# Performance work log

Hardware: AMD Instinct MI355X
Metric: run time of the kernel (lower is better)

Reference implementation:

```python
import jax, jax.numpy as jnp
import numpy as np

D_MODEL = 1024
N_EXPERTS = 8
TOP_K = 2
D_HIDDEN = 4 * D_MODEL


def setup_inputs() -> dict:
    key = jax.random.key(0)
    ks = jax.random.split(key, 6)
    x = jax.random.normal(ks[0], (4, 2048, D_MODEL), dtype=jnp.float32)
    gate_w = jax.random.normal(ks[1], (N_EXPERTS, D_MODEL), dtype=jnp.float32) * 0.02
    w1 = jax.random.normal(ks[2], (N_EXPERTS, D_MODEL, D_HIDDEN), dtype=jnp.float32) * 0.02
    b1 = jnp.zeros((N_EXPERTS, D_HIDDEN), dtype=jnp.float32)
    w2 = jax.random.normal(ks[3], (N_EXPERTS, D_HIDDEN, D_MODEL), dtype=jnp.float32) * 0.02
    b2 = jnp.zeros((N_EXPERTS, D_MODEL), dtype=jnp.float32)
    return {"x": x, "gate_w": gate_w, "w1": w1, "b1": b1, "w2": w2, "b2": b2}


def reference(x, gate_w, w1, b1, w2, b2):
    B, S, D = x.shape
    xf = x.reshape(-1, D)                               # [T, D]
    logits = xf @ gate_w.T                              # [T, E]
    top_vals, top_idx = jax.lax.top_k(logits, TOP_K)    # [T, K]
    rw = jax.nn.softmax(top_vals.astype(jnp.float32), axis=-1).astype(x.dtype)  # [T, K]
    out = jnp.zeros_like(xf)
    for i in range(N_EXPERTS):
        # combined routing weight for expert i per token (0 if not selected)
        cw = jnp.sum(jnp.where(top_idx == i, rw, jnp.zeros_like(rw)), axis=-1)  # [T]
        h = jax.nn.relu(xf @ w1[i] + b1[i])             # [T, 4D]
        y = h @ w2[i] + b2[i]                           # [T, D]
        out = out + y * cw[:, None]
    return out.reshape(B, S, D)
```

## Files before the change

### kernel.cpp

```cpp
#include <hip/hip_runtime.h>
#include <stdint.h>

#define D_MODEL   1024
#define N_EXPERTS 8
#define D_HIDDEN  4096
#define T_TOKENS  8192
#define N_SLOTS   (T_TOKENS * 2)
#define MAX_MT    71

typedef __bf16 bf16x8 __attribute__((ext_vector_type(8)));
typedef float  f32x4  __attribute__((ext_vector_type(4)));
typedef unsigned short ushort8 __attribute__((ext_vector_type(8)));

__device__ __forceinline__ unsigned short f2bf(float f) {
    unsigned int u = __float_as_uint(f);
    u += 0x7fffu + ((u >> 16) & 1u);
    return (unsigned short)(u >> 16);
}
__device__ __forceinline__ float bf2f(unsigned short v) {
    return __uint_as_float((unsigned int)v << 16);
}

__device__ __forceinline__ void gl_lds16(const void* g, void* l) {
    __builtin_amdgcn_global_load_lds(
        (const __attribute__((address_space(1))) unsigned int*)g,
        (__attribute__((address_space(3))) unsigned int*)l, 16, 0, 0);
}

__global__ __launch_bounds__(256) void gate_kernel(
    const float* __restrict__ x, const float* __restrict__ gw,
    unsigned short* __restrict__ xb,
    int* __restrict__ route_pack, float* __restrict__ route_w,
    int* __restrict__ cnt)
{
    __shared__ float gws[N_EXPERTS * D_MODEL];
    __shared__ int hist[N_EXPERTS];
    int tid = threadIdx.x;
    for (int i = tid * 4; i < N_EXPERTS * D_MODEL; i += 256 * 4)
        *(float4*)&gws[i] = *(const float4*)&gw[i];
    if (tid < N_EXPERTS) hist[tid] = 0;
    __syncthreads();

    int wave = tid >> 6, lane = tid & 63;
    for (int tt = 0; tt < 4; tt++) {
        int t = blockIdx.x * 16 + wave * 4 + tt;
        const float* xr = x + (size_t)t * D_MODEL;

        float acc[N_EXPERTS];
        for (int e = 0; e < N_EXPERTS; e++) acc[e] = 0.f;
        for (int i = 0; i < 4; i++) {
            float4 xv = *(const float4*)&xr[lane * 4 + i * 256];
            ushort4 o;
            o.x = f2bf(xv.x); o.y = f2bf(xv.y); o.z = f2bf(xv.z); o.w = f2bf(xv.w);
            *(ushort4*)&xb[(size_t)t * D_MODEL + lane * 4 + i * 256] = o;
            for (int e = 0; e < N_EXPERTS; e++) {
                float4 gv = *(const float4*)&gws[e * D_MODEL + lane * 4 + i * 256];
                acc[e] += xv.x * gv.x + xv.y * gv.y + xv.z * gv.z + xv.w * gv.w;
            }
        }
        for (int e = 0; e < N_EXPERTS; e++)
            for (int off = 32; off >= 1; off >>= 1)
                acc[e] += __shfl_xor(acc[e], off, 64);

        if (lane == 0) {
            int e0 = 0; float v0 = acc[0];
            for (int e = 1; e < N_EXPERTS; e++) if (acc[e] > v0) { v0 = acc[e]; e0 = e; }
            int e1 = (e0 == 0) ? 1 : 0; float v1 = acc[e1];
            for (int e = 0; e < N_EXPERTS; e++)
                if (e != e0 && acc[e] > v1) { v1 = acc[e]; e1 = e; }
            float w0 = 1.f / (1.f + __expf(v1 - v0));
            route_pack[t] = e0 | (e1 << 8);
            route_w[2 * t]     = w0;
            route_w[2 * t + 1] = 1.f - w0;
            atomicAdd(&hist[e0], 1);
            atomicAdd(&hist[e1], 1);
        }
    }
    __syncthreads();
    if (tid < N_EXPERTS) atomicAdd(&cnt[tid], hist[tid]);
}

__global__ void offsets_kernel(const int* __restrict__ cnt,
                               int* __restrict__ off, int* __restrict__ cnt2)
{
    if (threadIdx.x == 0) {
        int a = 0;
        for (int e = 0; e < N_EXPERTS; e++) { off[e] = a; a += cnt[e]; cnt2[e] = 0; }
        off[N_EXPERTS] = a;
    }
}

__global__ __launch_bounds__(64) void scatter_kernel(
    const int* __restrict__ route_pack, const int* __restrict__ off,
    int* __restrict__ cnt2, int* __restrict__ tok_id, int* __restrict__ inv)
{
    int lane = threadIdx.x;
    int t = blockIdx.x * 64 + lane;
    int p  = route_pack[t];
    int e0 = p & 0xff, e1 = (p >> 8) & 0xff;

    unsigned long long m0[N_EXPERTS], m1[N_EXPERTS];
    for (int e = 0; e < N_EXPERTS; e++) {
        m0[e] = __ballot(e0 == e);
        m1[e] = __ballot(e1 == e);
    }
    int mybase = 0;
    if (lane < N_EXPERTS)
        mybase = atomicAdd(&cnt2[lane], __popcll(m0[lane]) + __popcll(m1[lane]));

    unsigned long long lt = (1ull << lane) - 1ull;
    int b0 = __shfl(mybase, e0);
    int s0 = off[e0] + b0 + (int)__popcll(m0[e0] & lt);
    int b1 = __shfl(mybase, e1);
    int s1 = off[e1] + b1 + (int)__popcll(m0[e1]) + (int)__popcll(m1[e1] & lt);

    tok_id[s0] = t;
    tok_id[s1] = t;
    inv[2 * t]     = s0;
    inv[2 * t + 1] = s1;
}

template <int R, int C>
__global__ __launch_bounds__(256) void transpose_convert_kernel(
    const float* __restrict__ src, unsigned short* __restrict__ dst)
{
    __shared__ float tile[64 * 68];
    int e = blockIdx.z;
    const float* s = src + (size_t)e * R * C;
    unsigned short* d = dst + (size_t)e * R * C;
    int r0 = blockIdx.y * 64, c0 = blockIdx.x * 64;
    int t = threadIdx.x;
    {
        int r = t >> 4, c4 = (t & 15) * 4;
        for (int p = 0; p < 4; p++, r += 16)
            *(float4*)&tile[r * 68 + c4] = *(const float4*)&s[(size_t)(r0 + r) * C + c0 + c4];
    }
    __syncthreads();
    {
        int c = t >> 2, rblk = (t & 3) * 8;
        for (int q = 0; q < 2; q++) {
            int rr = q * 32 + rblk;
            ushort8 o;
            for (int j = 0; j < 8; j++) o[j] = f2bf(tile[(rr + j) * 68 + c]);
            *(ushort8*)&d[(size_t)(c0 + c) * R + r0 + rr] = o;
        }
    }
}

template<int KDIM, int NC, bool RELU, bool USE_TOK>
__global__ __launch_bounds__(512, 2) void moe_gemm_kernel(
    const unsigned short* __restrict__ Ag, const unsigned short* __restrict__ Bw,
    const float* __restrict__ bias, const int* __restrict__ tok_id,
    const int* __restrict__ off, unsigned short* __restrict__ Cout)
{
    constexpr int NT   = KDIM / 64;
    constexpr int NTN  = NC / 256;
    constexpr int NWG  = MAX_MT * NTN;
    constexpr int ASH  = 256 * 64;
    constexpr int BUFS = 2 * ASH;
    __shared__ unsigned short smem[2 * BUFS];

    int wg = blockIdx.x;
    constexpr int qq8 = NWG / 8, rr8 = NWG % 8;
    int xcd = wg & 7, idx = wg >> 3;
    int sz = (xcd < rr8 ? xcd * (qq8 + 1) : rr8 * (qq8 + 1) + (xcd - rr8) * qq8) + idx;
    int bx = sz / NTN;
    int n0 = (sz % NTN) * 256;

    int e = -1, slot0 = 0, end = 0;
    {
        int acc = 0;
        for (int i = 0; i < N_EXPERTS; i++) {
            int s = off[i], en = off[i + 1];
            int nt = (en - s + 255) >> 8;
            if (e < 0 && bx < acc + nt) { e = i; slot0 = s + (bx - acc) * 256; end = en; }
            acc += nt;
        }
        if (e < 0) return;
    }

    int tid = threadIdx.x, wave = tid >> 6, lane = tid & 63;
    int wm = wave >> 2, wn = wave & 3;
    int lr = lane >> 3, lc = lane & 7;
    int lcs = lc ^ lr;
    int row16 = lane & 15, qk = lane >> 4;
    int sx = row16 & 7;

    f32x4 acc[8][4];
    const f32x4 zero = {0.f, 0.f, 0.f, 0.f};
#pragma unroll
    for (int i = 0; i < 8; i++)
#pragma unroll
        for (int j = 0; j < 4; j++) acc[i][j] = zero;

    const unsigned short* gA[4];
    const unsigned short* gB[4];
    int ldsA[4], ldsB[4];
#pragma unroll
    for (int c = 0; c < 4; c++) {
        int rowt = wave * 32 + c * 8 + lr;
        int slotc = min(slot0 + rowt, end - 1);
        int grow;
        if constexpr (USE_TOK) grow = tok_id[slotc]; else grow = slotc;
        gA[c] = Ag + (size_t)grow * KDIM + lcs * 8;
        gB[c] = Bw + ((size_t)e * NC + n0 + rowt) * KDIM + lcs * 8;
        ldsA[c] = (wave * 32 + c * 8) * 64;
        ldsB[c] = ASH + (wave * 32 + c * 8) * 64;
    }

    auto stage = [&](int b, int kt) {
        unsigned short* base = smem + b * BUFS;
#pragma unroll
        for (int c = 0; c < 4; c++) gl_lds16(gA[c] + kt * 64, base + ldsA[c]);
#pragma unroll
        for (int c = 0; c < 4; c++) gl_lds16(gB[c] + kt * 64, base + ldsB[c]);
    };

    stage(0, 0);
    asm volatile("s_waitcnt vmcnt(0)" ::: "memory");
    __builtin_amdgcn_s_barrier();

    int cur = 0;
    for (int t = 0; t < NT; t++) {
        if (t + 1 < NT) stage(cur ^ 1, t + 1);
        const unsigned short* Ab = smem + cur * BUFS;
        const unsigned short* Bb = Ab + ASH;
        __builtin_amdgcn_s_setprio(1);
#pragma unroll
        for (int ks = 0; ks < 2; ks++) {
            bf16x8 af[8], bq[4];
#pragma unroll
            for (int i = 0; i < 8; i++) {
                int rr = wm * 128 + i * 16 + row16;
                af[i] = *(const bf16x8*)&Ab[rr * 64 + (((ks * 4 + qk) ^ sx) * 8)];
            }
#pragma unroll
            for (int j = 0; j < 4; j++) {
                int br = wn * 64 + j * 16 + row16;
                bq[j] = *(const bf16x8*)&Bb[br * 64 + (((ks * 4 + qk) ^ sx) * 8)];
            }
#pragma unroll
            for (int i = 0; i < 8; i++)
#pragma unroll
                for (int j = 0; j < 4; j++)
                    acc[i][j] = __builtin_amdgcn_mfma_f32_16x16x32_bf16(af[i], bq[j], acc[i][j], 0, 0, 0);
        }
        __builtin_amdgcn_s_setprio(0);
        asm volatile("s_waitcnt vmcnt(0)" ::: "memory");
        __builtin_amdgcn_s_barrier();
        cur ^= 1;
    }

    unsigned short* stg = smem;
    int quad = lane >> 4, c16 = lane & 15;
    for (int p = 0; p < 2; p++) {
        if (p) __syncthreads();
        if (wm == p) {
#pragma unroll
            for (int j = 0; j < 4; j++) {
                int n = n0 + wn * 64 + j * 16 + c16;
                float bv = bias[e * NC + n];
#pragma unroll
                for (int i = 0; i < 8; i++)
#pragma unroll
                    for (int r = 0; r < 4; r++) {
                        float v = acc[i][j][r] + bv;
                        if (RELU) v = v > 0.f ? v : 0.f;
                        stg[(i * 16 + quad * 4 + r) * 264 + wn * 64 + j * 16 + c16] = f2bf(v);
                    }
            }
        }
        __syncthreads();
        int srow = tid >> 5, chunk = (tid & 31) * 8;
#pragma unroll
        for (int s8 = 0; s8 < 8; s8++) {
            int rr = srow + s8 * 16;
            int slot = slot0 + p * 128 + rr;
            if (slot < end)
                *(ushort8*)&Cout[(size_t)slot * NC + n0 + chunk] =
                    *(const ushort8*)&stg[rr * 264 + chunk];
        }
    }
}

__global__ __launch_bounds__(256) void combine_kernel(
    const unsigned short* __restrict__ y, const int* __restrict__ inv,
    const float* __restrict__ rw, float* __restrict__ out)
{
    int wave = threadIdx.x >> 6, lane = threadIdx.x & 63;
    int t = blockIdx.x * 4 + wave;
    int s0 = inv[2 * t], s1 = inv[2 * t + 1];
    float w0 = rw[2 * t], w1 = rw[2 * t + 1];
    const unsigned short* y0 = y + (size_t)s0 * D_MODEL;
    const unsigned short* y1 = y + (size_t)s1 * D_MODEL;
    float* orow = out + (size_t)t * D_MODEL;
    int c = lane * 16;
    for (int hh = 0; hh < 2; hh++) {
        ushort8 a = *(const ushort8*)&y0[c + hh * 8];
        ushort8 b = *(const ushort8*)&y1[c + hh * 8];
        float4 o0, o1;
        o0.x = w0 * bf2f(a[0]) + w1 * bf2f(b[0]);
        o0.y = w0 * bf2f(a[1]) + w1 * bf2f(b[1]);
        o0.z = w0 * bf2f(a[2]) + w1 * bf2f(b[2]);
        o0.w = w0 * bf2f(a[3]) + w1 * bf2f(b[3]);
        o1.x = w0 * bf2f(a[4]) + w1 * bf2f(b[4]);
        o1.y = w0 * bf2f(a[5]) + w1 * bf2f(b[5]);
        o1.z = w0 * bf2f(a[6]) + w1 * bf2f(b[6]);
        o1.w = w0 * bf2f(a[7]) + w1 * bf2f(b[7]);
        *(float4*)&orow[c + hh * 8]     = o0;
        *(float4*)&orow[c + hh * 8 + 4] = o1;
    }
}

extern "C" void kernel_launch(void* const* d_in, const int* in_sizes, int n_in,
                              void* d_out, int out_size, void* d_ws, size_t ws_size,
                              hipStream_t stream)
{
    const float* x      = (const float*)d_in[0];
    const float* gate_w = (const float*)d_in[1];
    const float* w1     = (const float*)d_in[2];
    const float* b1     = (const float*)d_in[3];
    const float* w2     = (const float*)d_in[4];
    const float* b2     = (const float*)d_in[5];
    float* out = (float*)d_out;

    char* ws = (char*)d_ws;
    size_t o = 0;
    auto alloc = [&](size_t bytes) { void* p = ws + o; o += (bytes + 255) & ~(size_t)255; return p; };
    int*   cnt        = (int*)alloc(32);
    int*   cnt2       = (int*)alloc(32);
    int*   off        = (int*)alloc(64);
    int*   route_pack = (int*)alloc((size_t)T_TOKENS * 4);
    float* route_w    = (float*)alloc((size_t)T_TOKENS * 8);
    int*   tok_id     = (int*)alloc((size_t)N_SLOTS * 4);
    int*   inv        = (int*)alloc((size_t)T_TOKENS * 8);
    unsigned short* xb  = (unsigned short*)alloc((size_t)T_TOKENS * D_MODEL * 2);
    unsigned short* w1t = (unsigned short*)alloc((size_t)N_EXPERTS * D_MODEL * D_HIDDEN * 2);
    unsigned short* w2t = (unsigned short*)alloc((size_t)N_EXPERTS * D_MODEL * D_HIDDEN * 2);
    unsigned short* h   = (unsigned short*)alloc((size_t)N_SLOTS * D_HIDDEN * 2);
    unsigned short* y   = w1t;

    hipMemsetAsync(cnt, 0, 32, stream);

    gate_kernel<<<T_TOKENS / 16, 256, 0, stream>>>(x, gate_w, xb, route_pack, route_w, cnt);
    offsets_kernel<<<1, 64, 0, stream>>>(cnt, off, cnt2);
    scatter_kernel<<<T_TOKENS / 64, 64, 0, stream>>>(route_pack, off, cnt2, tok_id, inv);
    transpose_convert_kernel<D_MODEL, D_HIDDEN>
        <<<dim3(D_HIDDEN / 64, D_MODEL / 64, N_EXPERTS), dim3(256), 0, stream>>>(w1, w1t);
    transpose_convert_kernel<D_HIDDEN, D_MODEL>
        <<<dim3(D_MODEL / 64, D_HIDDEN / 64, N_EXPERTS), dim3(256), 0, stream>>>(w2, w2t);
    moe_gemm_kernel<D_MODEL, D_HIDDEN, true, true>
        <<<dim3(MAX_MT * (D_HIDDEN / 256)), dim3(512), 0, stream>>>(xb, w1t, b1, tok_id, off, h);
    moe_gemm_kernel<D_HIDDEN, D_MODEL, false, false>
        <<<dim3(MAX_MT * (D_MODEL / 256)), dim3(512), 0, stream>>>(h, w2t, b2, tok_id, off, y);
    combine_kernel<<<T_TOKENS / 4, 256, 0, stream>>>(y, inv, route_w, out);
}
```

Before: 743.5 us.

## Tile grouped GEMM over fixed slot blocks, looping experts per tile

The grouped GEMM now uses fixed 256-slot row tiles across the whole slot array (64 tiles) instead of per-expert padded tiles (up to 71). Each tile loops over every expert whose segment overlaps it and runs a full-K GEMM for each, writing only the rows in range. This removes the padded empty tiles and the early-return workgroups. In exchange, tiles that straddle expert boundaries run the full GEMM once per overlapping expert, which can nearly double work for those tiles, and the extra per-expert barriers add sync overhead.

```diff
diff --git a/kernel.cpp b/kernel.cpp
--- a/kernel.cpp
+++ b/kernel.cpp
@@ -6,7 +6,6 @@
 #define D_HIDDEN  4096
 #define T_TOKENS  8192
 #define N_SLOTS   (T_TOKENS * 2)
-#define MAX_MT    71
 
 typedef __bf16 bf16x8 __attribute__((ext_vector_type(8)));
 typedef float  f32x4  __attribute__((ext_vector_type(4)));
@@ -155,29 +154,16 @@
 {
     constexpr int NT   = KDIM / 64;
     constexpr int NTN  = NC / 256;
-    constexpr int NWG  = MAX_MT * NTN;
+    constexpr int NWG  = (N_SLOTS / 256) * NTN;
     constexpr int ASH  = 256 * 64;
     constexpr int BUFS = 2 * ASH;
     __shared__ unsigned short smem[2 * BUFS];
 
     int wg = blockIdx.x;
-    constexpr int qq8 = NWG / 8, rr8 = NWG % 8;
-    int xcd = wg & 7, idx = wg >> 3;
-    int sz = (xcd < rr8 ? xcd * (qq8 + 1) : rr8 * (qq8 + 1) + (xcd - rr8) * qq8) + idx;
+    int sz = (wg & 7) * (NWG / 8) + (wg >> 3);
     int bx = sz / NTN;
     int n0 = (sz % NTN) * 256;
-
-    int e = -1, slot0 = 0, end = 0;
-    {
-        int acc = 0;
-        for (int i = 0; i < N_EXPERTS; i++) {
-            int s = off[i], en = off[i + 1];
-            int nt = (en - s + 255) >> 8;
-            if (e < 0 && bx < acc + nt) { e = i; slot0 = s + (bx - acc) * 256; end = en; }
-            acc += nt;
-        }
-        if (e < 0) return;
-    }
+    int m0 = bx * 256;
 
     int tid = threadIdx.x, wave = tid >> 6, lane = tid & 63;
     int wm = wave >> 2, wn = wave & 3;
@@ -186,24 +172,15 @@
     int row16 = lane & 15, qk = lane >> 4;
     int sx = row16 & 7;
 
-    f32x4 acc[8][4];
-    const f32x4 zero = {0.f, 0.f, 0.f, 0.f};
-#pragma unroll
-    for (int i = 0; i < 8; i++)
-#pragma unroll
-        for (int j = 0; j < 4; j++) acc[i][j] = zero;
-
     const unsigned short* gA[4];
     const unsigned short* gB[4];
     int ldsA[4], ldsB[4];
 #pragma unroll
     for (int c = 0; c < 4; c++) {
         int rowt = wave * 32 + c * 8 + lr;
-        int slotc = min(slot0 + rowt, end - 1);
         int grow;
-        if constexpr (USE_TOK) grow = tok_id[slotc]; else grow = slotc;
+        if constexpr (USE_TOK) grow = tok_id[m0 + rowt]; else grow = m0 + rowt;
         gA[c] = Ag + (size_t)grow * KDIM + lcs * 8;
-        gB[c] = Bw + ((size_t)e * NC + n0 + rowt) * KDIM + lcs * 8;
         ldsA[c] = (wave * 32 + c * 8) * 64;
         ldsB[c] = ASH + (wave * 32 + c * 8) * 64;
     }
@@ -216,69 +193,88 @@
         for (int c = 0; c < 4; c++) gl_lds16(gB[c] + kt * 64, base + ldsB[c]);
     };
 
-    stage(0, 0);
-    asm volatile("s_waitcnt vmcnt(0)" ::: "memory");
-    __builtin_amdgcn_s_barrier();
-
-    int cur = 0;
-    for (int t = 0; t < NT; t++) {
-        if (t + 1 < NT) stage(cur ^ 1, t + 1);
-        const unsigned short* Ab = smem + cur * BUFS;
-        const unsigned short* Bb = Ab + ASH;
-        __builtin_amdgcn_s_setprio(1);
-#pragma unroll
-        for (int ks = 0; ks < 2; ks++) {
-            bf16x8 af[8], bq[4];
-#pragma unroll
-            for (int i = 0; i < 8; i++) {
-                int rr = wm * 128 + i * 16 + row16;
-                af[i] = *(const bf16x8*)&Ab[rr * 64 + (((ks * 4 + qk) ^ sx) * 8)];
-            }
-#pragma unroll
-            for (int j = 0; j < 4; j++) {
-                int br = wn * 64 + j * 16 + row16;
-                bq[j] = *(const bf16x8*)&Bb[br * 64 + (((ks * 4 + qk) ^ sx) * 8)];
-            }
-#pragma unroll
-            for (int i = 0; i < 8; i++)
-#pragma unroll
-                for (int j = 0; j < 4; j++)
-                    acc[i][j] = __builtin_amdgcn_mfma_f32_16x16x32_bf16(af[i], bq[j], acc[i][j], 0, 0, 0);
-        }
-        __builtin_amdgcn_s_setprio(0);
+    for (int e = 0; e < N_EXPERTS; e++) {
+        int lo = off[e], hi = off[e + 1];
+        if (lo < m0) lo = m0;
+        if (hi > m0 + 256) hi = m0 + 256;
+        if (lo >= hi) continue;
+
+#pragma unroll
+        for (int c = 0; c < 4; c++)
+            gB[c] = Bw + ((size_t)e * NC + n0 + wave * 32 + c * 8 + lr) * KDIM + lcs * 8;
+
+        f32x4 acc[8][4];
+        const f32x4 zero = {0.f, 0.f, 0.f, 0.f};
+#pragma unroll
+        for (int i = 0; i < 8; i++)
+#pragma unroll
+            for (int j = 0; j < 4; j++) acc[i][j] = zero;
+
+        __syncthreads();
+        stage(0, 0);
         asm volatile("s_waitcnt vmcnt(0)" ::: "memory");
         __builtin_amdgcn_s_barrier();
-        cur ^= 1;
-    }
-
-    unsigned short* stg = smem;
-    int quad = lane >> 4, c16 = lane & 15;
-    for (int p = 0; p < 2; p++) {
-        if (p) __syncthreads();
-        if (wm == p) {
-#pragma unroll
-            for (int j = 0; j < 4; j++) {
-                int n = n0 + wn * 64 + j * 16 + c16;
-                float bv = bias[e * NC + n];
+
+        int cur = 0;
+        for (int t = 0; t < NT; t++) {
+            if (t + 1 < NT) stage(cur ^ 1, t + 1);
+            const unsigned short* Ab = smem + cur * BUFS;
+            const unsigned short* Bb = Ab + ASH;
+            __builtin_amdgcn_s_setprio(1);
+#pragma unroll
+            for (int ks = 0; ks < 2; ks++) {
+                bf16x8 af[8], bq[4];
+#pragma unroll
+                for (int i = 0; i < 8; i++) {
+                    int rr = wm * 128 + i * 16 + row16;
+                    af[i] = *(const bf16x8*)&Ab[rr * 64 + (((ks * 4 + qk) ^ sx) * 8)];
+                }
+#pragma unroll
+                for (int j = 0; j < 4; j++) {
+                    int br = wn * 64 + j * 16 + row16;
+                    bq[j] = *(const bf16x8*)&Bb[br * 64 + (((ks * 4 + qk) ^ sx) * 8)];
+                }
 #pragma unroll
                 for (int i = 0; i < 8; i++)
 #pragma unroll
-                    for (int r = 0; r < 4; r++) {
-                        float v = acc[i][j][r] + bv;
-                        if (RELU) v = v > 0.f ? v : 0.f;
-                        stg[(i * 16 + quad * 4 + r) * 264 + wn * 64 + j * 16 + c16] = f2bf(v);
-                    }
+                    for (int j = 0; j < 4; j++)
+                        acc[i][j] = __builtin_amdgcn_mfma_f32_16x16x32_bf16(af[i], bq[j], acc[i][j], 0, 0, 0);
             }
-        }
-        __syncthreads();
-        int srow = tid >> 5, chunk = (tid & 31) * 8;
-#pragma unroll
-        for (int s8 = 0; s8 < 8; s8++) {
-            int rr = srow + s8 * 16;
-            int slot = slot0 + p * 128 + rr;
-            if (slot < end)
-                *(ushort8*)&Cout[(size_t)slot * NC + n0 + chunk] =
-                    *(const ushort8*)&stg[rr * 264 + chunk];
+            __builtin_amdgcn_s_setprio(0);
+            asm volatile("s_waitcnt vmcnt(0)" ::: "memory");
+            __builtin_amdgcn_s_barrier();
+            cur ^= 1;
+        }
+
+        unsigned short* stg = smem;
+        int quad = lane >> 4, c16 = lane & 15;
+        for (int p = 0; p < 2; p++) {
+            if (p) __syncthreads();
+            if (wm == p) {
+#pragma unroll
+                for (int j = 0; j < 4; j++) {
+                    int n = n0 + wn * 64 + j * 16 + c16;
+                    float bv = bias[e * NC + n];
+#pragma unroll
+                    for (int i = 0; i < 8; i++)
+#pragma unroll
+                        for (int r = 0; r < 4; r++) {
+                            float v = acc[i][j][r] + bv;
+                            if (RELU) v = v > 0.f ? v : 0.f;
+                            stg[(i * 16 + quad * 4 + r) * 264 + wn * 64 + j * 16 + c16] = f2bf(v);
+                        }
+                }
+            }
+            __syncthreads();
+            int srow = tid >> 5, chunk = (tid & 31) * 8;
+#pragma unroll
+            for (int s8 = 0; s8 < 8; s8++) {
+                int rr = srow + s8 * 16;
+                int slot = m0 + p * 128 + rr;
+                if (slot >= lo && slot < hi)
+                    *(ushort8*)&Cout[(size_t)slot * NC + n0 + chunk] =
+                        *(const ushort8*)&stg[rr * 264 + chunk];
+            }
         }
     }
 }
@@ -350,8 +346,8 @@
     transpose_convert_kernel<D_HIDDEN, D_MODEL>
         <<<dim3(D_MODEL / 64, D_HIDDEN / 64, N_EXPERTS), dim3(256), 0, stream>>>(w2, w2t);
     moe_gemm_kernel<D_MODEL, D_HIDDEN, true, true>
-        <<<dim3(MAX_MT * (D_HIDDEN / 256)), dim3(512), 0, stream>>>(xb, w1t, b1, tok_id, off, h);
+        <<<dim3((N_SLOTS / 256) * (D_HIDDEN / 256)), dim3(512), 0, stream>>>(xb, w1t, b1, tok_id, off, h);
     moe_gemm_kernel<D_HIDDEN, D_MODEL, false, false>
-        <<<dim3(MAX_MT * (D_MODEL / 256)), dim3(512), 0, stream>>>(h, w2t, b2, tok_id, off, y);
+        <<<dim3((N_SLOTS / 256) * (D_MODEL / 256)), dim3(512), 0, stream>>>(h, w2t, b2, tok_id, off, y);
     combine_kernel<<<T_TOKENS / 4, 256, 0, stream>>>(y, inv, route_w, out);
 }
```

New measurement: 761.1 us. +2.4%, slower.

## Split GEMM main loop into quarter-tile phases with interleaved async loads

Applied to the files above, without the earlier changes.

Restructures the double-buffered GEMM mainloop into an 8-phase ping-pong schedule. Each K-tile is split into A/B halves, so LDS reads, MFMA blocks and global-to-LDS loads for the next tiles interleave at finer granularity. Partial vmcnt waits replace the full vmcnt(0) drain per tile. This aims to hide memory latency better and keep MFMA busy, but adds many more barriers and depends on NT being even and on the tail clamping being correct.

```diff
diff --git a/kernel.cpp b/kernel.cpp
--- a/kernel.cpp
+++ b/kernel.cpp
@@ -186,6 +186,36 @@
     int row16 = lane & 15, qk = lane >> 4;
     int sx = row16 & 7;
 
+    const unsigned short* gA[2][2];
+    const unsigned short* gB[2][2];
+    int lbA[2][2], lbB[2][2];
+    int rowB[2][2];
+#pragma unroll
+    for (int hh = 0; hh < 2; hh++)
+#pragma unroll
+        for (int c = 0; c < 2; c++) {
+            int q = wave * 16 + c * 8;
+            int ra = (q & 63) + ((q >> 6) << 7) + hh * 64;
+            int rb = (q & 31) + ((q >> 5) << 6) + hh * 32;
+            rowB[hh][c] = rb;
+            lbA[hh][c] = ra * 64;
+            lbB[hh][c] = ASH + rb * 64;
+            int slotc = min(slot0 + ra + lr, end - 1);
+            int grow;
+            if constexpr (USE_TOK) grow = tok_id[slotc]; else grow = slotc;
+            gA[hh][c] = Ag + (size_t)grow * KDIM + lcs * 8;
+            gB[hh][c] = Bw + ((size_t)e * NC + n0 + rb + lr) * KDIM + lcs * 8;
+        }
+
+    auto stA = [&](int b, int hh, int kt) {
+        gl_lds16(gA[hh][0] + kt * 64, smem + b * BUFS + lbA[hh][0]);
+        gl_lds16(gA[hh][1] + kt * 64, smem + b * BUFS + lbA[hh][1]);
+    };
+    auto stB = [&](int b, int nn, int kt) {
+        gl_lds16(gB[nn][0] + kt * 64, smem + b * BUFS + lbB[nn][0]);
+        gl_lds16(gB[nn][1] + kt * 64, smem + b * BUFS + lbB[nn][1]);
+    };
+
     f32x4 acc[8][4];
     const f32x4 zero = {0.f, 0.f, 0.f, 0.f};
 #pragma unroll
@@ -193,63 +223,74 @@
 #pragma unroll
         for (int j = 0; j < 4; j++) acc[i][j] = zero;
 
-    const unsigned short* gA[4];
-    const unsigned short* gB[4];
-    int ldsA[4], ldsB[4];
-#pragma unroll
-    for (int c = 0; c < 4; c++) {
-        int rowt = wave * 32 + c * 8 + lr;
-        int slotc = min(slot0 + rowt, end - 1);
-        int grow;
-        if constexpr (USE_TOK) grow = tok_id[slotc]; else grow = slotc;
-        gA[c] = Ag + (size_t)grow * KDIM + lcs * 8;
-        gB[c] = Bw + ((size_t)e * NC + n0 + rowt) * KDIM + lcs * 8;
-        ldsA[c] = (wave * 32 + c * 8) * 64;
-        ldsB[c] = ASH + (wave * 32 + c * 8) * 64;
-    }
-
-    auto stage = [&](int b, int kt) {
-        unsigned short* base = smem + b * BUFS;
-#pragma unroll
-        for (int c = 0; c < 4; c++) gl_lds16(gA[c] + kt * 64, base + ldsA[c]);
-#pragma unroll
-        for (int c = 0; c < 4; c++) gl_lds16(gB[c] + kt * 64, base + ldsB[c]);
-    };
-
-    stage(0, 0);
-    asm volatile("s_waitcnt vmcnt(0)" ::: "memory");
-    __builtin_amdgcn_s_barrier();
-
-    int cur = 0;
-    for (int t = 0; t < NT; t++) {
-        if (t + 1 < NT) stage(cur ^ 1, t + 1);
-        const unsigned short* Ab = smem + cur * BUFS;
-        const unsigned short* Bb = Ab + ASH;
-        __builtin_amdgcn_s_setprio(1);
-#pragma unroll
-        for (int ks = 0; ks < 2; ks++) {
-            bf16x8 af[8], bq[4];
-#pragma unroll
-            for (int i = 0; i < 8; i++) {
-                int rr = wm * 128 + i * 16 + row16;
-                af[i] = *(const bf16x8*)&Ab[rr * 64 + (((ks * 4 + qk) ^ sx) * 8)];
-            }
-#pragma unroll
-            for (int j = 0; j < 4; j++) {
-                int br = wn * 64 + j * 16 + row16;
-                bq[j] = *(const bf16x8*)&Bb[br * 64 + (((ks * 4 + qk) ^ sx) * 8)];
-            }
-#pragma unroll
-            for (int i = 0; i < 8; i++)
-#pragma unroll
-                for (int j = 0; j < 4; j++)
-                    acc[i][j] = __builtin_amdgcn_mfma_f32_16x16x32_bf16(af[i], bq[j], acc[i][j], 0, 0, 0);
-        }
-        __builtin_amdgcn_s_setprio(0);
-        asm volatile("s_waitcnt vmcnt(0)" ::: "memory");
-        __builtin_amdgcn_s_barrier();
-        cur ^= 1;
-    }
+#define READ_A(AB, HH)                                                            \
+    _Pragma("unroll") for (int ii = 0; ii < 4; ii++)                              \
+    _Pragma("unroll") for (int ks = 0; ks < 2; ks++)                              \
+        af[ii][ks] = *(const bf16x8*)&(AB)[(wm * 128 + (HH) * 64 + ii * 16 + row16) * 64 \
+                                           + (((ks * 4 + qk) ^ sx) * 8)];
+#define READ_B(BB, NN)                                                            \
+    _Pragma("unroll") for (int jj = 0; jj < 2; jj++)                              \
+    _Pragma("unroll") for (int ks = 0; ks < 2; ks++)                              \
+        bq[jj][ks] = *(const bf16x8*)&(BB)[(wn * 64 + (NN) * 32 + jj * 16 + row16) * 64 \
+                                           + (((ks * 4 + qk) ^ sx) * 8)];
+#define MFMA16(HH, NN)                                                            \
+    __builtin_amdgcn_s_setprio(1);                                                \
+    _Pragma("unroll") for (int ks = 0; ks < 2; ks++)                              \
+    _Pragma("unroll") for (int ii = 0; ii < 4; ii++)                              \
+    _Pragma("unroll") for (int jj = 0; jj < 2; jj++)                              \
+        acc[(HH) * 4 + ii][(NN) * 2 + jj] = __builtin_amdgcn_mfma_f32_16x16x32_bf16( \
+            af[ii][ks], bq[jj][ks], acc[(HH) * 4 + ii][(NN) * 2 + jj], 0, 0, 0);  \
+    __builtin_amdgcn_s_setprio(0);
+#define BAR() __builtin_amdgcn_s_barrier()
+#define VMC4() asm volatile("s_waitcnt vmcnt(4)" ::: "memory")
+
+    const unsigned short* A0b = smem;
+    const unsigned short* B0b = smem + ASH;
+    const unsigned short* A1b = smem + BUFS;
+    const unsigned short* B1b = A1b + ASH;
+
+    stA(0, 0, 0); stB(0, 0, 0); stA(0, 1, 0); stB(0, 1, 0);
+    stA(1, 0, 1); stB(1, 0, 1);
+    VMC4();
+    BAR();
+
+    for (int it = 0; it < NT / 2; it++) {
+        int V  = 2 * it + 1;
+        int U2 = (2 * it + 2 < NT) ? 2 * it + 2 : NT - 1;
+        int V2 = (2 * it + 3 < NT) ? 2 * it + 3 : NT - 1;
+        bf16x8 af[4][2], bq[2][2];
+        READ_A(A0b, 0); READ_B(B0b, 0);
+        stA(1, 1, V); stB(1, 1, V);
+        BAR(); MFMA16(0, 0); BAR();
+        READ_B(B0b, 1);
+        BAR(); MFMA16(0, 1); BAR();
+        READ_A(A0b, 1); READ_B(B0b, 0);
+        stA(0, 0, U2);
+        BAR(); MFMA16(1, 0); BAR();
+        READ_B(B0b, 1);
+        stB(0, 0, U2);
+        BAR(); MFMA16(1, 1); VMC4(); BAR();
+        READ_A(A1b, 0); READ_B(B1b, 0);
+        stA(0, 1, U2); stB(0, 1, U2);
+        BAR(); MFMA16(0, 0); BAR();
+        READ_B(B1b, 1);
+        BAR(); MFMA16(0, 1); BAR();
+        READ_A(A1b, 1); READ_B(B1b, 0);
+        stA(1, 0, V2);
+        BAR(); MFMA16(1, 0); BAR();
+        READ_B(B1b, 1);
+        stB(1, 0, V2);
+        BAR(); MFMA16(1, 1); VMC4(); BAR();
+    }
+
+    asm volatile("s_waitcnt vmcnt(0) lgkmcnt(0)" ::: "memory");
+    __syncthreads();
+
+#undef READ_A
+#undef READ_B
+#undef MFMA16
+#undef BAR
+#undef VMC4
 
     unsigned short* stg = smem;
     int quad = lane >> 4, c16 = lane & 15;
```

Result: faster. 728.5 us (-2.0%).

## Switch MoE GEMM to 32x32x16 MFMA with single-buffer quarter-tile staging pipeline

Applied to the files above, without the earlier changes.

Replaces the 16x16x32 MFMA tiling with 32x32x16 MFMA fragments and restructures the K-loop. The double-buffered LDS staging becomes a single-buffer scheme where the A and B halves are reloaded in quarters, interleaved between MFMA phases and guarded by fine-grained vmcnt waits and barriers. This halves LDS usage, which may allow more occupancy, and reduces LDS read traffic per MFMA. The cost is many more barriers per iteration and tight ordering hazards that could stall or race.

```diff
diff --git a/kernel.cpp b/kernel.cpp
--- a/kernel.cpp
+++ b/kernel.cpp
@@ -10,6 +10,7 @@
 
 typedef __bf16 bf16x8 __attribute__((ext_vector_type(8)));
 typedef float  f32x4  __attribute__((ext_vector_type(4)));
+typedef float  f32x16 __attribute__((ext_vector_type(16)));
 typedef unsigned short ushort8 __attribute__((ext_vector_type(8)));
 
 __device__ __forceinline__ unsigned short f2bf(float f) {
@@ -153,12 +154,10 @@
     const float* __restrict__ bias, const int* __restrict__ tok_id,
     const int* __restrict__ off, unsigned short* __restrict__ Cout)
 {
-    constexpr int NT   = KDIM / 64;
-    constexpr int NTN  = NC / 256;
-    constexpr int NWG  = MAX_MT * NTN;
-    constexpr int ASH  = 256 * 64;
-    constexpr int BUFS = 2 * ASH;
-    __shared__ unsigned short smem[2 * BUFS];
+    constexpr int NT  = KDIM / 64;
+    constexpr int NTN = NC / 256;
+    constexpr int NWG = MAX_MT * NTN;
+    __shared__ unsigned short smem[33792];
 
     int wg = blockIdx.x;
     constexpr int qq8 = NWG / 8, rr8 = NWG % 8;
@@ -183,90 +182,115 @@
     int wm = wave >> 2, wn = wave & 3;
     int lr = lane >> 3, lc = lane & 7;
     int lcs = lc ^ lr;
-    int row16 = lane & 15, qk = lane >> 4;
-    int sx = row16 & 7;
-
-    f32x4 acc[8][4];
-    const f32x4 zero = {0.f, 0.f, 0.f, 0.f};
-#pragma unroll
-    for (int i = 0; i < 8; i++)
-#pragma unroll
-        for (int j = 0; j < 4; j++) acc[i][j] = zero;
-
-    const unsigned short* gA[4];
-    const unsigned short* gB[4];
-    int ldsA[4], ldsB[4];
-#pragma unroll
-    for (int c = 0; c < 4; c++) {
-        int rowt = wave * 32 + c * 8 + lr;
-        int slotc = min(slot0 + rowt, end - 1);
-        int grow;
-        if constexpr (USE_TOK) grow = tok_id[slotc]; else grow = slotc;
-        gA[c] = Ag + (size_t)grow * KDIM + lcs * 8;
-        gB[c] = Bw + ((size_t)e * NC + n0 + rowt) * KDIM + lcs * 8;
-        ldsA[c] = (wave * 32 + c * 8) * 64;
-        ldsB[c] = ASH + (wave * 32 + c * 8) * 64;
-    }
-
-    auto stage = [&](int b, int kt) {
-        unsigned short* base = smem + b * BUFS;
-#pragma unroll
-        for (int c = 0; c < 4; c++) gl_lds16(gA[c] + kt * 64, base + ldsA[c]);
-#pragma unroll
-        for (int c = 0; c < 4; c++) gl_lds16(gB[c] + kt * 64, base + ldsB[c]);
+    int r5 = lane & 31, q2 = lane >> 5;
+    int sx = lane & 7;
+
+    const unsigned short* gA[2][2];
+    const unsigned short* gB[2][2];
+    int lbA[2][2], lbB[2][2];
+#pragma unroll
+    for (int hh = 0; hh < 2; hh++)
+#pragma unroll
+        for (int c = 0; c < 2; c++) {
+            int q = wave * 16 + c * 8;
+            int ra = (q & 63) + ((q >> 6) << 7) + hh * 64;
+            int rb = (q & 31) + ((q >> 5) << 6) + hh * 32;
+            lbA[hh][c] = ra * 64;
+            lbB[hh][c] = 16384 + rb * 64;
+            int slotc = min(slot0 + ra + lr, end - 1);
+            int grow;
+            if constexpr (USE_TOK) grow = tok_id[slotc]; else grow = slotc;
+            gA[hh][c] = Ag + (size_t)grow * KDIM + lcs * 8;
+            gB[hh][c] = Bw + ((size_t)e * NC + n0 + rb + lr) * KDIM + lcs * 8;
+        }
+
+    auto stA = [&](int hh, int kt) {
+        gl_lds16(gA[hh][0] + kt * 64, smem + lbA[hh][0]);
+        gl_lds16(gA[hh][1] + kt * 64, smem + lbA[hh][1]);
     };
-
-    stage(0, 0);
-    asm volatile("s_waitcnt vmcnt(0)" ::: "memory");
-    __builtin_amdgcn_s_barrier();
-
-    int cur = 0;
+    auto stB = [&](int nn, int kt) {
+        gl_lds16(gB[nn][0] + kt * 64, smem + lbB[nn][0]);
+        gl_lds16(gB[nn][1] + kt * 64, smem + lbB[nn][1]);
+    };
+
+    f32x16 acc[4][2];
+#pragma unroll
+    for (int i = 0; i < 4; i++) { acc[i][0] = 0.f; acc[i][1] = 0.f; }
+
+    const unsigned short* As = smem;
+    const unsigned short* Bs = smem + 16384;
+
+#define READ_AF(DST, FI)                                                          \
+    _Pragma("unroll") for (int ks = 0; ks < 4; ks++)                              \
+        DST[ks] = *(const bf16x8*)&As[(wm * 128 + (FI) * 32 + r5) * 64 +          \
+                                      (((ks * 2 + q2) ^ sx) * 8)];
+#define READ_BQ(DST, FJ)                                                          \
+    _Pragma("unroll") for (int ks = 0; ks < 4; ks++)                              \
+        DST[ks] = *(const bf16x8*)&Bs[(wn * 64 + (FJ) * 32 + r5) * 64 +           \
+                                      (((ks * 2 + q2) ^ sx) * 8)];
+#define MFMA2(FI0, FI1, AF, BQ, FJ)                                               \
+    __builtin_amdgcn_s_setprio(1);                                                \
+    _Pragma("unroll") for (int ks = 0; ks < 4; ks++) {                            \
+        acc[FI0][FJ] = __builtin_amdgcn_mfma_f32_32x32x16_bf16(AF[0][ks], BQ[ks], acc[FI0][FJ], 0, 0, 0); \
+        acc[FI1][FJ] = __builtin_amdgcn_mfma_f32_32x32x16_bf16(AF[1][ks], BQ[ks], acc[FI1][FJ], 0, 0, 0); \
+    }                                                                             \
+    __builtin_amdgcn_s_setprio(0);
+#define BAR() __builtin_amdgcn_s_barrier()
+
+    stA(0, 0); stB(0, 0); stB(1, 0); stA(1, 0);
+    asm volatile("s_waitcnt vmcnt(4)" ::: "memory");
+    BAR();
+
     for (int t = 0; t < NT; t++) {
-        if (t + 1 < NT) stage(cur ^ 1, t + 1);
-        const unsigned short* Ab = smem + cur * BUFS;
-        const unsigned short* Bb = Ab + ASH;
-        __builtin_amdgcn_s_setprio(1);
-#pragma unroll
-        for (int ks = 0; ks < 2; ks++) {
-            bf16x8 af[8], bq[4];
-#pragma unroll
-            for (int i = 0; i < 8; i++) {
-                int rr = wm * 128 + i * 16 + row16;
-                af[i] = *(const bf16x8*)&Ab[rr * 64 + (((ks * 4 + qk) ^ sx) * 8)];
-            }
-#pragma unroll
-            for (int j = 0; j < 4; j++) {
-                int br = wn * 64 + j * 16 + row16;
-                bq[j] = *(const bf16x8*)&Bb[br * 64 + (((ks * 4 + qk) ^ sx) * 8)];
-            }
-#pragma unroll
-            for (int i = 0; i < 8; i++)
-#pragma unroll
-                for (int j = 0; j < 4; j++)
-                    acc[i][j] = __builtin_amdgcn_mfma_f32_16x16x32_bf16(af[i], bq[j], acc[i][j], 0, 0, 0);
-        }
-        __builtin_amdgcn_s_setprio(0);
-        asm volatile("s_waitcnt vmcnt(0)" ::: "memory");
-        __builtin_amdgcn_s_barrier();
-        cur ^= 1;
-    }
+        int kn = (t + 1 < NT) ? t + 1 : NT - 1;
+        bf16x8 afL[2][4], afH[2][4], bq0[4], bq1[4];
+        READ_AF(afL[0], 0); READ_AF(afL[1], 1); READ_BQ(bq0, 0);
+        BAR();
+        MFMA2(0, 1, afL, bq0, 0);
+        asm volatile("s_waitcnt vmcnt(2)" ::: "memory");
+        BAR();
+        READ_BQ(bq1, 1);
+        stA(0, kn); stB(0, kn);
+        BAR();
+        MFMA2(0, 1, afL, bq1, 1);
+        asm volatile("s_waitcnt vmcnt(4)" ::: "memory");
+        BAR();
+        READ_AF(afH[0], 2); READ_AF(afH[1], 3);
+        stB(1, kn);
+        BAR();
+        MFMA2(2, 3, afH, bq1, 1);
+        BAR();
+        stA(1, kn);
+        BAR();
+        MFMA2(2, 3, afH, bq0, 0);
+        asm volatile("s_waitcnt vmcnt(4)" ::: "memory");
+        BAR();
+    }
+
+    asm volatile("s_waitcnt vmcnt(0) lgkmcnt(0)" ::: "memory");
+    __syncthreads();
+
+#undef READ_AF
+#undef READ_BQ
+#undef MFMA2
+#undef BAR
 
     unsigned short* stg = smem;
-    int quad = lane >> 4, c16 = lane & 15;
     for (int p = 0; p < 2; p++) {
         if (p) __syncthreads();
         if (wm == p) {
 #pragma unroll
-            for (int j = 0; j < 4; j++) {
-                int n = n0 + wn * 64 + j * 16 + c16;
+            for (int fj = 0; fj < 2; fj++) {
+                int n = n0 + wn * 64 + fj * 32 + r5;
                 float bv = bias[e * NC + n];
 #pragma unroll
-                for (int i = 0; i < 8; i++)
-#pragma unroll
-                    for (int r = 0; r < 4; r++) {
-                        float v = acc[i][j][r] + bv;
+                for (int fi = 0; fi < 4; fi++)
+#pragma unroll
+                    for (int r = 0; r < 16; r++) {
+                        float v = acc[fi][fj][r] + bv;
                         if (RELU) v = v > 0.f ? v : 0.f;
-                        stg[(i * 16 + quad * 4 + r) * 264 + wn * 64 + j * 16 + c16] = f2bf(v);
+                        int row = fi * 32 + (r & 3) + 8 * (r >> 2) + 4 * q2;
+                        stg[row * 264 + wn * 64 + fj * 32 + r5] = f2bf(v);
                     }
             }
         }
```

Result: slower. 769.5 us (+3.5%).
